# Kernel optimization log

Measured on AMD Instinct MI355X. Metric: run time of the kernel, lower is better.

## Reference

```python
import jax, jax.numpy as jnp
import numpy as np

B, C, H, W = 8, 512, 96, 96
CK, CV, K = 64, 64, 3  # key/value channels = C/8, kernel_size=3


def setup_inputs() -> dict:
    key = jax.random.key(0)
    ks = jax.random.split(key, 11)
    p = lambda k, shape: jax.random.normal(k, shape, dtype=jnp.float32) * 0.05
    return {
        "x": jax.random.normal(ks[0], (B, C, H, W), dtype=jnp.float32),
        "key1_w": p(ks[1], (CK, C, 1, 1)),
        "key1_b": p(ks[2], (CK,)),
        "key_dw_w": p(ks[3], (CK, 1, K, K)),
        "key_dw_b": p(ks[4], (CK,)),
        "key3_w": p(ks[5], (K * K, CK, 1, 1)),
        "key3_b": p(ks[6], (K * K,)),
        "value_w": p(ks[7], (CV, C, 1, 1)),
        "value_b": p(ks[8], (CV,)),
        "out_w": p(ks[9], (C, CV, 1, 1)),
        "out_b": p(ks[10], (C,)),
    }


def _conv1x1(x, w, b):
    # x: [B,Cin,H,W], w: [Cout,Cin,1,1]
    return jnp.einsum('bchw,oc->bohw', x, w[:, :, 0, 0]) + b[None, :, None, None]


def _unfold3(x):
    # nn.Unfold(kernel_size=3, stride=1, padding=1) then view -> [B,C,9,H,W]
    b, c, h, w = x.shape
    xp = jnp.pad(x, ((0, 0), (0, 0), (1, 1), (1, 1)))
    patches = [xp[:, :, i:i + h, j:j + w] for i in range(3) for j in range(3)]
    return jnp.stack(patches, axis=2)  # [B,C,9,H,W], row-major kernel order like torch


def reference(x, key1_w, key1_b, key_dw_w, key_dw_b, key3_w, key3_b,
              value_w, value_b, out_w, out_b):
    # key branch: 1x1 conv + ReLU -> depthwise 3x3 (no act) -> 1x1 -> k^2 logits
    k = jax.nn.relu(_conv1x1(x, key1_w, key1_b))
    k = jax.lax.conv_general_dilated(
        k, key_dw_w, window_strides=(1, 1), padding='SAME',
        feature_group_count=CK,
        dimension_numbers=('NCHW', 'OIHW', 'NCHW')) + key_dw_b[None, :, None, None]
    k = _conv1x1(k, key3_w, key3_b)            # [B,9,H,W]
    weights = jax.nn.softmax(k[:, None], axis=2)  # [B,1,9,H,W], softmax over kernel taps

    # value branch: 1x1 conv (no act) then unfold 3x3 neighborhoods
    v = _unfold3(_conv1x1(x, value_w, value_b))   # [B,CV,9,H,W]

    y = jnp.sum(weights * v, axis=2)              # [B,CV,H,W]
    return x + _conv1x1(y, out_w, out_b)
```

## Files before the change

### kernel.cpp

```cpp
#include <hip/hip_runtime.h>

#define B_ 8
#define C_ 512
#define H_ 96
#define W_ 96
#define HW_ (H_ * W_)
#define CK_ 64

typedef __attribute__((ext_vector_type(8))) short bf16x8;
typedef __attribute__((ext_vector_type(4))) float f32x4;

__device__ __forceinline__ short f2bf(float f) {
    union { float f; unsigned u; } v; v.f = f;
    unsigned r = v.u + 0x7fffu + ((v.u >> 16) & 1u);
    return (short)(r >> 16);
}

__device__ __forceinline__ bf16x8 cvt8(float4 a, float4 b) {
    bf16x8 s;
    s[0] = f2bf(a.x); s[1] = f2bf(a.y); s[2] = f2bf(a.z); s[3] = f2bf(a.w);
    s[4] = f2bf(b.x); s[5] = f2bf(b.y); s[6] = f2bf(b.z); s[7] = f2bf(b.w);
    return s;
}


__global__ __launch_bounds__(256, 4)
void kv_conv_mfma(const float* __restrict__ x,
                  const float* __restrict__ key1_w, const float* __restrict__ key1_b,
                  const float* __restrict__ value_w, const float* __restrict__ value_b,
                  float* __restrict__ outbuf)
{
    const int b    = blockIdx.y;
    const int px0  = blockIdx.x * 128;
    const int tid  = threadIdx.x;
    const int lane = tid & 63;
    const int w    = tid >> 6;
    const int wm   = w & 1;
    const int wn   = w >> 1;
    const int l15  = lane & 15;
    const int q    = lane >> 4;

    __shared__ short  Ws[128][40];
    __shared__ float  s_bias[128];

    if (tid < 128) s_bias[tid] = (tid < 64) ? key1_b[tid] : value_b[tid - 64];

    f32x4 acc[4][4];
#pragma unroll
    for (int i = 0; i < 4; ++i)
#pragma unroll
        for (int j = 0; j < 4; ++j) acc[i][j] = (f32x4){0.f, 0.f, 0.f, 0.f};

    const float* xb = x + (size_t)b * C_ * HW_ + px0;

    const int wrow_i = tid >> 1;
    const int c16    = (tid & 1) * 16;
    const float* wrow = (wrow_i < 64) ? (key1_w + wrow_i * C_)
                                      : (value_w + (wrow_i - 64) * C_);

    for (int kc = 0; kc < C_; kc += 32) {
        __syncthreads();
        {
            const float* wp = wrow + kc + c16;
            float4 f0 = *(const float4*)(wp);
            float4 f1 = *(const float4*)(wp + 4);
            float4 f2 = *(const float4*)(wp + 8);
            float4 f3 = *(const float4*)(wp + 12);
            *(bf16x8*)&Ws[wrow_i][c16]     = cvt8(f0, f1);
            *(bf16x8*)&Ws[wrow_i][c16 + 8] = cvt8(f2, f3);
        }
        __syncthreads();

        bf16x8 af[4];
#pragma unroll
        for (int mt = 0; mt < 4; ++mt)
            af[mt] = *(bf16x8*)&Ws[wm * 64 + mt * 16 + l15][q * 8];

        const float* xq = xb + (size_t)(kc + q * 8) * HW_ + wn * 64 + l15;
#pragma unroll
        for (int nt = 0; nt < 4; ++nt) {
            const float* xp = xq + nt * 16;
            bf16x8 bf;
#pragma unroll
            for (int j = 0; j < 8; ++j) bf[j] = f2bf(xp[(size_t)j * HW_]);
#pragma unroll
            for (int mt = 0; mt < 4; ++mt)
                acc[mt][nt] = __builtin_amdgcn_mfma_f32_16x16x32_bf16(af[mt], bf, acc[mt][nt], 0, 0, 0);
        }
    }

    float* kvb = outbuf + ((size_t)b * C_ + 64) * HW_ + px0;
#pragma unroll
    for (int mt = 0; mt < 4; ++mt) {
#pragma unroll
        for (int r = 0; r < 4; ++r) {
            int oc = wm * 64 + mt * 16 + q * 4 + r;
            float bias = s_bias[oc];
#pragma unroll
            for (int nt = 0; nt < 4; ++nt) {
                float v = acc[mt][nt][r] + bias;
                if (oc < 64) v = fmaxf(v, 0.f);
                kvb[(size_t)oc * HW_ + wn * 64 + nt * 16 + l15] = v;
            }
        }
    }
}

__global__ __launch_bounds__(256, 4)
void attn_kernel(const float* __restrict__ dw_w, const float* __restrict__ dw_b,
                 const float* __restrict__ k3_w, const float* __restrict__ k3_b,
                 float* __restrict__ outbuf)
{
    const int b  = blockIdx.y;
    const int hw = blockIdx.x * 256 + threadIdx.x;
    const int h  = hw / W_;
    const int w  = hw % W_;

    __shared__ float s_dw[CK_ * 9];
    __shared__ float s_dwb[CK_];
    __shared__ float s_k3[9 * CK_];
    __shared__ float s_k3b[16];

    for (int i = threadIdx.x; i < CK_ * 9; i += 256) {
        s_dw[i] = dw_w[i];
        s_k3[i] = k3_w[i];
    }
    if (threadIdx.x < CK_) s_dwb[threadIdx.x] = dw_b[threadIdx.x];
    if (threadIdx.x < 9)   s_k3b[threadIdx.x] = k3_b[threadIdx.x];
    __syncthreads();

    int  off[9];
    bool valid[9];
#pragma unroll
    for (int t = 0; t < 9; ++t) {
        int dy = t / 3 - 1, dx = t % 3 - 1;
        int hh = h + dy, ww = w + dx;
        valid[t] = (hh >= 0) && (hh < H_) && (ww >= 0) && (ww < W_);
        off[t]   = hh * W_ + ww;
    }

    float logits[9];
#pragma unroll
    for (int t = 0; t < 9; ++t) logits[t] = s_k3b[t];

    const float* kb = outbuf + ((size_t)b * C_ + 64) * HW_;
#pragma unroll 4
    for (int c = 0; c < CK_; ++c) {
        const float* kc = kb + (size_t)c * HW_;
        float d = s_dwb[c];
#pragma unroll
        for (int t = 0; t < 9; ++t) {
            float val = valid[t] ? kc[off[t]] : 0.f;
            d = fmaf(s_dw[c * 9 + t], val, d);
        }
#pragma unroll
        for (int t = 0; t < 9; ++t)
            logits[t] = fmaf(s_k3[t * CK_ + c], d, logits[t]);
    }

    float m = logits[0];
#pragma unroll
    for (int t = 1; t < 9; ++t) m = fmaxf(m, logits[t]);
    float e[9], s = 0.f;
#pragma unroll
    for (int t = 0; t < 9; ++t) { e[t] = __expf(logits[t] - m); s += e[t]; }
    float inv = 1.f / s;
    float wt[9];
#pragma unroll
    for (int t = 0; t < 9; ++t) wt[t] = e[t] * inv;

    const float* vb = kb + (size_t)CK_ * HW_;
    float* yb = outbuf + (size_t)b * C_ * HW_;
#pragma unroll 4
    for (int cv = 0; cv < CK_; ++cv) {
        const float* vc = vb + (size_t)cv * HW_;
        float acc = 0.f;
#pragma unroll
        for (int t = 0; t < 9; ++t) {
            float val = valid[t] ? vc[off[t]] : 0.f;
            acc = fmaf(wt[t], val, acc);
        }
        yb[(size_t)cv * HW_ + hw] = acc;
    }
}

__global__ __launch_bounds__(256, 4)
void out_conv_mfma(const float* __restrict__ out_w, const float* __restrict__ out_b,
                   const float* __restrict__ x, float* outbuf, int oc_base)
{
    const int b    = blockIdx.z;
    const int o0   = oc_base + blockIdx.y * 128;
    const int px0  = blockIdx.x * 128;
    const int tid  = threadIdx.x;
    const int lane = tid & 63;
    const int w    = tid >> 6;
    const int wm   = w & 1;
    const int wn   = w >> 1;
    const int l15  = lane & 15;
    const int q    = lane >> 4;

    __shared__ short Ws[128][72];
    __shared__ float s_bias[128];

    {
        int row = tid & 127, half = tid >> 7;
        const float* wp = out_w + (size_t)(o0 + row) * CK_ + half * 32;
        float4 f0 = *(const float4*)(wp);
        float4 f1 = *(const float4*)(wp + 4);
        float4 f2 = *(const float4*)(wp + 8);
        float4 f3 = *(const float4*)(wp + 12);
        float4 f4 = *(const float4*)(wp + 16);
        float4 f5 = *(const float4*)(wp + 20);
        float4 f6 = *(const float4*)(wp + 24);
        float4 f7 = *(const float4*)(wp + 28);
        *(bf16x8*)&Ws[row][half * 32]      = cvt8(f0, f1);
        *(bf16x8*)&Ws[row][half * 32 + 8]  = cvt8(f2, f3);
        *(bf16x8*)&Ws[row][half * 32 + 16] = cvt8(f4, f5);
        *(bf16x8*)&Ws[row][half * 32 + 24] = cvt8(f6, f7);
    }
    if (tid < 128) s_bias[tid] = out_b[o0 + tid];
    __syncthreads();

    f32x4 acc[4][4];
#pragma unroll
    for (int i = 0; i < 4; ++i)
#pragma unroll
        for (int j = 0; j < 4; ++j) acc[i][j] = (f32x4){0.f, 0.f, 0.f, 0.f};

    const float* yb = outbuf + (size_t)b * C_ * HW_ + px0;

#pragma unroll
    for (int kc = 0; kc < CK_; kc += 32) {
        bf16x8 af[4];
#pragma unroll
        for (int mt = 0; mt < 4; ++mt)
            af[mt] = *(bf16x8*)&Ws[wm * 64 + mt * 16 + l15][kc + q * 8];

        const float* yq = yb + (size_t)(kc + q * 8) * HW_ + wn * 64 + l15;
#pragma unroll
        for (int nt = 0; nt < 4; ++nt) {
            const float* yp = yq + nt * 16;
            bf16x8 bf;
#pragma unroll
            for (int j = 0; j < 8; ++j) bf[j] = f2bf(yp[(size_t)j * HW_]);
#pragma unroll
            for (int mt = 0; mt < 4; ++mt)
                acc[mt][nt] = __builtin_amdgcn_mfma_f32_16x16x32_bf16(af[mt], bf, acc[mt][nt], 0, 0, 0);
        }
    }

    __syncthreads();

    const float* xb = x + (size_t)b * C_ * HW_ + px0;
    float* ob       = outbuf + (size_t)b * C_ * HW_ + px0;
#pragma unroll
    for (int mt = 0; mt < 4; ++mt) {
#pragma unroll
        for (int r = 0; r < 4; ++r) {
            int ol   = wm * 64 + mt * 16 + q * 4 + r;
            int oc   = o0 + ol;
            float bias = s_bias[ol];
#pragma unroll
            for (int nt = 0; nt < 4; ++nt) {
                size_t idx = (size_t)oc * HW_ + wn * 64 + nt * 16 + l15;
                ob[idx] = acc[mt][nt][r] + bias + xb[idx];
            }
        }
    }
}

extern "C" void kernel_launch(void* const* d_in, const int* in_sizes, int n_in,
                              void* d_out, int out_size, void* d_ws, size_t ws_size,
                              hipStream_t stream)
{
    const float* x       = (const float*)d_in[0];
    const float* key1_w  = (const float*)d_in[1];
    const float* key1_b  = (const float*)d_in[2];
    const float* dw_w    = (const float*)d_in[3];
    const float* dw_b    = (const float*)d_in[4];
    const float* k3_w    = (const float*)d_in[5];
    const float* k3_b    = (const float*)d_in[6];
    const float* value_w = (const float*)d_in[7];
    const float* value_b = (const float*)d_in[8];
    const float* out_w   = (const float*)d_in[9];
    const float* out_b   = (const float*)d_in[10];
    float* out = (float*)d_out;

    dim3 g1(HW_ / 128, B_);
    kv_conv_mfma<<<g1, dim3(256), 0, stream>>>(x, key1_w, key1_b, value_w, value_b, out);

    dim3 g2(HW_ / 256, B_);
    attn_kernel<<<g2, dim3(256), 0, stream>>>(dw_w, dw_b, k3_w, k3_b, out);

    dim3 g3(HW_ / 128, 3, B_);
    out_conv_mfma<<<g3, dim3(256), 0, stream>>>(out_w, out_b, x, out, 128);

    dim3 g4(HW_ / 128, 1, B_);
    out_conv_mfma<<<g4, dim3(256), 0, stream>>>(out_w, out_b, x, out, 0);
}
```

Measured before the change: 467.4 us.

## Pre-pack bf16 weights in a separate kernel and halve kv-conv pixel tile

Adds a small kernel that converts key1/value weights to bf16 once, in an MFMA-fragment-friendly layout, and stores them in a spare region of the output buffer. The kv conv kernel then reads A fragments straight from global memory, with no per-iteration LDS staging or barriers. The pixel tile per block also drops from 128 to 64, which doubles the grid. The cost is an extra launch, a reliance on scratch space in the output buffer being free at that point, and redundant global reads of the weight fragments from every block.

```diff
diff --git a/kernel.cpp b/kernel.cpp
--- a/kernel.cpp
+++ b/kernel.cpp
@@ -10,6 +10,8 @@
 typedef __attribute__((ext_vector_type(8))) short bf16x8;
 typedef __attribute__((ext_vector_type(4))) float f32x4;
 
+#define WPK_OFF ((size_t)192 * HW_)
+
 __device__ __forceinline__ short f2bf(float f) {
     union { float f; unsigned u; } v; v.f = f;
     unsigned r = v.u + 0x7fffu + ((v.u >> 16) & 1u);
@@ -24,14 +26,29 @@
 }
 
 
+__global__ void pack_w_kernel(const float* __restrict__ key1_w,
+                              const float* __restrict__ value_w,
+                              float* __restrict__ outbuf)
+{
+    const int idx = blockIdx.x * 256 + threadIdx.x;
+    const int c8  = idx >> 7;
+    const int oc  = idx & 127;
+    const float* src = (oc < 64) ? (key1_w + (size_t)oc * C_)
+                                 : (value_w + (size_t)(oc - 64) * C_);
+    float4 f0 = *(const float4*)(src + c8 * 8);
+    float4 f1 = *(const float4*)(src + c8 * 8 + 4);
+    short* wpk = (short*)(outbuf + WPK_OFF);
+    *(bf16x8*)(wpk + (size_t)idx * 8) = cvt8(f0, f1);
+}
+
 __global__ __launch_bounds__(256, 4)
 void kv_conv_mfma(const float* __restrict__ x,
-                  const float* __restrict__ key1_w, const float* __restrict__ key1_b,
-                  const float* __restrict__ value_w, const float* __restrict__ value_b,
+                  const float* __restrict__ key1_b,
+                  const float* __restrict__ value_b,
                   float* __restrict__ outbuf)
 {
     const int b    = blockIdx.y;
-    const int px0  = blockIdx.x * 128;
+    const int px0  = blockIdx.x * 64;
     const int tid  = threadIdx.x;
     const int lane = tid & 63;
     const int w    = tid >> 6;
@@ -40,46 +57,30 @@
     const int l15  = lane & 15;
     const int q    = lane >> 4;
 
-    __shared__ short  Ws[128][40];
-    __shared__ float  s_bias[128];
-
+    __shared__ float s_bias[128];
     if (tid < 128) s_bias[tid] = (tid < 64) ? key1_b[tid] : value_b[tid - 64];
-
-    f32x4 acc[4][4];
+    __syncthreads();
+
+    f32x4 acc[4][2];
 #pragma unroll
     for (int i = 0; i < 4; ++i)
 #pragma unroll
-        for (int j = 0; j < 4; ++j) acc[i][j] = (f32x4){0.f, 0.f, 0.f, 0.f};
-
-    const float* xb = x + (size_t)b * C_ * HW_ + px0;
-
-    const int wrow_i = tid >> 1;
-    const int c16    = (tid & 1) * 16;
-    const float* wrow = (wrow_i < 64) ? (key1_w + wrow_i * C_)
-                                      : (value_w + (wrow_i - 64) * C_);
-
-    for (int kc = 0; kc < C_; kc += 32) {
-        __syncthreads();
-        {
-            const float* wp = wrow + kc + c16;
-            float4 f0 = *(const float4*)(wp);
-            float4 f1 = *(const float4*)(wp + 4);
-            float4 f2 = *(const float4*)(wp + 8);
-            float4 f3 = *(const float4*)(wp + 12);
-            *(bf16x8*)&Ws[wrow_i][c16]     = cvt8(f0, f1);
-            *(bf16x8*)&Ws[wrow_i][c16 + 8] = cvt8(f2, f3);
-        }
-        __syncthreads();
-
+        for (int j = 0; j < 2; ++j) acc[i][j] = (f32x4){0.f, 0.f, 0.f, 0.f};
+
+    const short* wpk = (const short*)(outbuf + WPK_OFF);
+    const short* apk = wpk + ((size_t)q * 128 + wm * 64 + l15) * 8;
+    const float* xq  = x + (size_t)b * C_ * HW_ + (size_t)(q * 8) * HW_
+                         + px0 + wn * 32 + l15;
+
+    for (int i = 0; i < 16; ++i) {
         bf16x8 af[4];
 #pragma unroll
         for (int mt = 0; mt < 4; ++mt)
-            af[mt] = *(bf16x8*)&Ws[wm * 64 + mt * 16 + l15][q * 8];
-
-        const float* xq = xb + (size_t)(kc + q * 8) * HW_ + wn * 64 + l15;
-#pragma unroll
-        for (int nt = 0; nt < 4; ++nt) {
-            const float* xp = xq + nt * 16;
+            af[mt] = *(const bf16x8*)(apk + ((size_t)i * 512 + mt * 16) * 8);
+
+#pragma unroll
+        for (int nt = 0; nt < 2; ++nt) {
+            const float* xp = xq + (size_t)i * 32 * HW_ + nt * 16;
             bf16x8 bf;
 #pragma unroll
             for (int j = 0; j < 8; ++j) bf[j] = f2bf(xp[(size_t)j * HW_]);
@@ -97,10 +98,10 @@
             int oc = wm * 64 + mt * 16 + q * 4 + r;
             float bias = s_bias[oc];
 #pragma unroll
-            for (int nt = 0; nt < 4; ++nt) {
+            for (int nt = 0; nt < 2; ++nt) {
                 float v = acc[mt][nt][r] + bias;
                 if (oc < 64) v = fmaxf(v, 0.f);
-                kvb[(size_t)oc * HW_ + wn * 64 + nt * 16 + l15] = v;
+                kvb[(size_t)oc * HW_ + wn * 32 + nt * 16 + l15] = v;
             }
         }
     }
@@ -286,8 +287,10 @@
     const float* out_b   = (const float*)d_in[10];
     float* out = (float*)d_out;
 
-    dim3 g1(HW_ / 128, B_);
-    kv_conv_mfma<<<g1, dim3(256), 0, stream>>>(x, key1_w, key1_b, value_w, value_b, out);
+    pack_w_kernel<<<dim3(32), dim3(256), 0, stream>>>(key1_w, value_w, out);
+
+    dim3 g1(HW_ / 64, B_);
+    kv_conv_mfma<<<g1, dim3(256), 0, stream>>>(x, key1_b, value_b, out);
 
     dim3 g2(HW_ / 256, B_);
     attn_kernel<<<g2, dim3(256), 0, stream>>>(dw_w, dw_b, k3_w, k3_b, out);
```

Result: no change. 474.0 us (+1.4%).
